# Kernel optimization log

Measured on AMD Instinct MI355X. Metric: run time of the kernel, lower is better.

## Reference

```python
import jax, jax.numpy as jnp
import numpy as np

D, H, DH, DFF, K = 512, 8, 64, 2048, 31
B, T = 8, 1024


def _ln(x, g, b):
    m = x.mean(-1, keepdims=True)
    v = ((x - m) ** 2).mean(-1, keepdims=True)
    return (x - m) / jnp.sqrt(v + 1e-5) * g + b


def _silu(x):
    return x * jax.nn.sigmoid(x)


def _pe(t, d):
    i = jnp.arange(t, dtype=jnp.float32)[:, None]
    j = jnp.arange(0, d, 2, dtype=jnp.float32)
    ang = i * (1.0 / (10000.0 ** (j / d)))
    pe = jnp.zeros((t, d), jnp.float32)
    pe = pe.at[:, 0::2].set(jnp.sin(ang))
    pe = pe.at[:, 1::2].set(jnp.cos(ang))
    return pe


def setup_inputs() -> dict:
    key = jax.random.key(0)
    ks = iter(jax.random.split(key, 40))
    s = 0.02
    d = {
        'x': jax.random.normal(next(ks), (B, T, D), jnp.float32),
        # FF module 1
        'ff1_ln_g': jnp.ones((D,), jnp.float32), 'ff1_ln_b': jnp.zeros((D,), jnp.float32),
        'ff1_w1': jax.random.normal(next(ks), (D, DFF), jnp.float32) * s,
        'ff1_b1': jnp.zeros((DFF,), jnp.float32),
        'ff1_w2': jax.random.normal(next(ks), (DFF, D), jnp.float32) * s,
        'ff1_b2': jnp.zeros((D,), jnp.float32),
        # MHSA
        'mha_ln_g': jnp.ones((D,), jnp.float32), 'mha_ln_b': jnp.zeros((D,), jnp.float32),
        'wq': jax.random.normal(next(ks), (H, D, DH), jnp.float32) * s,
        'bq': jnp.zeros((H, DH), jnp.float32),
        'wk': jax.random.normal(next(ks), (H, D, DH), jnp.float32) * s,
        'bk': jnp.zeros((H, DH), jnp.float32),
        'wv': jax.random.normal(next(ks), (H, D, DH), jnp.float32) * s,
        'bv': jnp.zeros((H, DH), jnp.float32),
        'wo': jax.random.normal(next(ks), (D, D), jnp.float32) * s,
        'bo': jnp.zeros((D,), jnp.float32),
        # Conv module
        'cv_ln_g': jnp.ones((D,), jnp.float32), 'cv_ln_b': jnp.zeros((D,), jnp.float32),
        'cv_w1': jax.random.normal(next(ks), (2 * D, D), jnp.float32) * s,
        'cv_b1': jnp.zeros((2 * D,), jnp.float32),
        'cv_wd': jax.random.normal(next(ks), (D, D, K), jnp.float32) * s,
        'cv_bn_g': jnp.ones((D,), jnp.float32), 'cv_bn_b': jnp.zeros((D,), jnp.float32),
        'cv_w2': jax.random.normal(next(ks), (D, D), jnp.float32) * s,
        'cv_b2': jnp.zeros((D,), jnp.float32),
        # FF module 2
        'ff2_ln_g': jnp.ones((D,), jnp.float32), 'ff2_ln_b': jnp.zeros((D,), jnp.float32),
        'ff2_w1': jax.random.normal(next(ks), (D, DFF), jnp.float32) * s,
        'ff2_b1': jnp.zeros((DFF,), jnp.float32),
        'ff2_w2': jax.random.normal(next(ks), (DFF, D), jnp.float32) * s,
        'ff2_b2': jnp.zeros((D,), jnp.float32),
        # final layer norm
        'fin_g': jnp.ones((D,), jnp.float32), 'fin_b': jnp.zeros((D,), jnp.float32),
    }
    return d


def _block(x, p):
    def ffn(x, g, b, w1, b1, w2, b2):
        y = _silu(_ln(x, g, b) @ w1 + b1) @ w2 + b2
        return x + y  # FeedForwardModule internal residual

    # x = x + 0.5 * ff_1(x)
    x = x + 0.5 * ffn(x, p['ff1_ln_g'], p['ff1_ln_b'], p['ff1_w1'], p['ff1_b1'], p['ff1_w2'], p['ff1_b2'])

    # MHSA module (with its own internal residual), then block residual
    y = _ln(x, p['mha_ln_g'], p['mha_ln_b']) + _pe(x.shape[1], x.shape[2])
    q = jnp.einsum('btd,hde->bhte', y, p['wq']) + p['bq'][None, :, None, :]
    k = jnp.einsum('btd,hde->bhte', y, p['wk']) + p['bk'][None, :, None, :]
    v = jnp.einsum('btd,hde->bhte', y, p['wv']) + p['bv'][None, :, None, :]
    scores = jnp.einsum('bhtd,bhsd->bhts', q, k) * (1.0 / np.sqrt(DH))
    attn = jax.nn.softmax(scores, axis=-1)
    o = jnp.einsum('bhts,bhsd->bhtd', attn, v)
    # faithful to original: raw view [B,H,T,dh] -> [B,T,H*dh] (no transpose)
    o = o.reshape(x.shape[0], x.shape[1], H * DH)
    o = o @ p['wo'] + p['bo']
    x = x + (x + o)

    # Convolution module (internal residual), then block residual
    y = _ln(x, p['cv_ln_g'], p['cv_ln_b']).swapaxes(1, 2)  # [B,D,T]
    y = jnp.einsum('ed,bdt->bet', p['cv_w1'], y) + p['cv_b1'][None, :, None]
    a, g = jnp.split(y, 2, axis=1)
    y = a * jax.nn.sigmoid(g)  # GLU over channel dim
    y = jax.lax.conv_general_dilated(y, p['cv_wd'], (1,), [(K // 2, K // 2)],
                                     dimension_numbers=('NCH', 'OIH', 'NCH'))
    # BatchNorm1d in training mode: batch stats over (batch, time), biased variance
    m = y.mean((0, 2), keepdims=True)
    var = ((y - m) ** 2).mean((0, 2), keepdims=True)
    y = (y - m) / jnp.sqrt(var + 1e-5) * p['cv_bn_g'][None, :, None] + p['cv_bn_b'][None, :, None]
    y = _silu(y)
    y = jnp.einsum('ed,bdt->bet', p['cv_w2'], y) + p['cv_b2'][None, :, None]
    y = y.swapaxes(1, 2)
    x = x + (x + y)

    # x = x + 0.5 * ff_2(x)
    x = x + 0.5 * ffn(x, p['ff2_ln_g'], p['ff2_ln_b'], p['ff2_w1'], p['ff2_b1'], p['ff2_w2'], p['ff2_b2'])

    return _ln(x, p['fin_g'], p['fin_b'])


def reference(x, ff1_ln_g, ff1_ln_b, ff1_w1, ff1_b1, ff1_w2, ff1_b2,
              mha_ln_g, mha_ln_b, wq, bq, wk, bk, wv, bv, wo, bo,
              cv_ln_g, cv_ln_b, cv_w1, cv_b1, cv_wd, cv_bn_g, cv_bn_b, cv_w2, cv_b2,
              ff2_ln_g, ff2_ln_b, ff2_w1, ff2_b1, ff2_w2, ff2_b2,
              fin_g, fin_b):
    p = dict(ff1_ln_g=ff1_ln_g, ff1_ln_b=ff1_ln_b, ff1_w1=ff1_w1, ff1_b1=ff1_b1,
             ff1_w2=ff1_w2, ff1_b2=ff1_b2, mha_ln_g=mha_ln_g, mha_ln_b=mha_ln_b,
             wq=wq, bq=bq, wk=wk, bk=bk, wv=wv, bv=bv, wo=wo, bo=bo,
             cv_ln_g=cv_ln_g, cv_ln_b=cv_ln_b, cv_w1=cv_w1, cv_b1=cv_b1, cv_wd=cv_wd,
             cv_bn_g=cv_bn_g, cv_bn_b=cv_bn_b, cv_w2=cv_w2, cv_b2=cv_b2,
             ff2_ln_g=ff2_ln_g, ff2_ln_b=ff2_ln_b, ff2_w1=ff2_w1, ff2_b1=ff2_b1,
             ff2_w2=ff2_w2, ff2_b2=ff2_b2, fin_g=fin_g, fin_b=fin_b)
    return _block(x, p)
```

## Files before the change

kernel.cpp:

```cpp
#include <hip/hip_runtime.h>


typedef __attribute__((ext_vector_type(4))) float f32x4;
typedef __attribute__((ext_vector_type(8))) short short8;
typedef __attribute__((ext_vector_type(4))) short s16x4;

__device__ __forceinline__ float bfs2f(short s) {
  unsigned u = ((unsigned)(unsigned short)s) << 16;
  float f; __builtin_memcpy(&f, &u, 4); return f;
}
__device__ __forceinline__ short f2bfs(float f) {
  unsigned u; __builtin_memcpy(&u, &f, 4);
  u = (u + 0x7FFFu + ((u >> 16) & 1u)) >> 16;
  return (short)u;
}
__device__ __forceinline__ float sigmoidf_(float x) { return 1.f / (1.f + __expf(-x)); }

#define GLOADLDS(gsrc, ldst) \
  __builtin_amdgcn_global_load_lds((__attribute__((address_space(1))) void*)(gsrc), \
                                   (__attribute__((address_space(3))) void*)(ldst), 16, 0, 0)

#define VMCNT_ASM(n) asm volatile("s_waitcnt vmcnt(" #n ")" ::: "memory")
template<int N> __device__ __forceinline__ void vmcnt_wait() {
  if      constexpr (N == 0)  VMCNT_ASM(0);
  else if constexpr (N == 2)  VMCNT_ASM(2);
  else if constexpr (N == 3)  VMCNT_ASM(3);
  else if constexpr (N == 4)  VMCNT_ASM(4);
  else if constexpr (N == 6)  VMCNT_ASM(6);
  else if constexpr (N == 8)  VMCNT_ASM(8);
  else                        VMCNT_ASM(0);
}
#define MEMFENCE asm volatile("" ::: "memory")

enum { EPI_SILU = 0, EPI_F32BIAS = 1, EPI_RES = 2, EPI_QKV = 3, EPI_F32 = 6 };

template<int BM, int BN, int WM, int WN, int EPI>
__global__ __launch_bounds__(256) void gemm_bt(
    const short* __restrict__ A, int lda, long zAh, long zAl,
    const short* __restrict__ BT, int ldbt, long zBh, long zBl,
    int K, int Kdec,
    void* C, int ldc, long zCh, long zCl, int zdiv,
    const float* bias, const float* bias2, const float* bias3,
    const float* resid, float alpha, float beta)
{
  constexpr int FM = BM / (WM * 16), FN = BN / (WN * 16);
  constexpr int AIT = (BM * 4) / 256, BIT = (BN * 4) / 256;
  constexpr int L = AIT + BIT;
  __shared__ short sA[3][BM * 32];
  __shared__ short sB[3][BN * 32];
  const int tid = threadIdx.x;
  const int zmask = (1 << zdiv) - 1;
  const int zhi = (int)(blockIdx.z >> zdiv);
  const int zlo = (int)(blockIdx.z & zmask);
  A  += (long)zhi * zAh + (long)zlo * zAl;
  BT += (long)zhi * zBh + (long)zlo * zBl;
  char* cbase = (char*)C + (long)zhi * zCh + (long)zlo * zCl;
  const int m0 = blockIdx.x * BM, n0 = blockIdx.y * BN;
  const int Keff = K - (zlo == zmask ? Kdec : 0);

  auto stage = [&](int buf, int k0) {
#pragma unroll
    for (int it = 0; it < AIT; ++it) {
      int idx = it * 256 + tid;
      GLOADLDS(A + (long)(m0 + (idx >> 2)) * lda + k0 + (idx & 3) * 8, &sA[buf][idx * 8]);
    }
#pragma unroll
    for (int it = 0; it < BIT; ++it) {
      int idx = it * 256 + tid;
      GLOADLDS(BT + (long)(n0 + (idx >> 2)) * ldbt + k0 + (idx & 3) * 8, &sB[buf][idx * 8]);
    }
  };

  f32x4 acc[FM][FN];
#pragma unroll
  for (int i = 0; i < FM; ++i) {
#pragma unroll
    for (int j = 0; j < FN; ++j) acc[i][j] = (f32x4){0.f, 0.f, 0.f, 0.f};
  }
  const int lane = tid & 63, wid = tid >> 6;
  const int wm = wid / WN, wn = wid % WN;
  const int lr = lane & 15, kg = lane >> 4;
  const int aRow = wm * (BM / WM), bRow = wn * (BN / WN);

  const int nt = Keff >> 5;
  stage(0, 0);
  stage(1, 32);
  vmcnt_wait<L>();
  __builtin_amdgcn_s_barrier();

  int cur = 0, sbuf = 2;
  for (int t = 0; t < nt; ++t) {
    const bool st = (t + 2 < nt);
    if (st) stage(sbuf, (t + 2) * 32);
    short8 af[FM], bfr[FN];
#pragma unroll
    for (int mi = 0; mi < FM; ++mi)
      af[mi] = *(const short8*)&sA[cur][(aRow + mi * 16 + lr) * 32 + kg * 8];
#pragma unroll
    for (int ni = 0; ni < FN; ++ni)
      bfr[ni] = *(const short8*)&sB[cur][(bRow + ni * 16 + lr) * 32 + kg * 8];
#pragma unroll
    for (int mi = 0; mi < FM; ++mi) {
#pragma unroll
      for (int ni = 0; ni < FN; ++ni)
        acc[mi][ni] = __builtin_amdgcn_mfma_f32_16x16x32_bf16(af[mi], bfr[ni], acc[mi][ni], 0, 0, 0);
    }
    if (st) vmcnt_wait<L>(); else vmcnt_wait<0>();
    __builtin_amdgcn_s_barrier();
    cur = (cur == 2) ? 0 : cur + 1;
    sbuf = (sbuf == 2) ? 0 : sbuf + 1;
  }

  const int baseRow = m0 + aRow, baseCol = n0 + bRow;
#pragma unroll
  for (int mi = 0; mi < FM; ++mi) {
#pragma unroll
    for (int ni = 0; ni < FN; ++ni) {
      const int col = baseCol + ni * 16 + lr;
#pragma unroll
      for (int r = 0; r < 4; ++r) {
        const int row = baseRow + mi * 16 + kg * 4 + r;
        float v = acc[mi][ni][r];
        if (EPI == EPI_SILU) {
          v += bias[col];
          v = v * sigmoidf_(v);
          ((short*)cbase)[(long)row * ldc + col] = f2bfs(v);
        } else if (EPI == EPI_F32BIAS) {
          v += bias[col];
          ((float*)cbase)[(long)row * ldc + col] = v;
        } else if (EPI == EPI_RES) {
          v += bias[col];
          float rv = resid[(long)row * ldc + col];
          ((float*)cbase)[(long)row * ldc + col] = alpha * rv + beta * v;
        } else if (EPI == EPI_QKV) {
          if (col < 512)       v = (v + bias[col]) * 0.125f;
          else if (col < 1024) v += bias2[col - 512];
          else                 v += bias3[col - 1024];
          ((short*)cbase)[(long)row * ldc + col] = f2bfs(v);
        } else if (EPI == EPI_F32) {
          ((float*)cbase)[(long)row * ldc + col] = v;
        }
      }
    }
  }
}

__global__ __launch_bounds__(256) void conv_tap(
    const short* __restrict__ glu,
    const short* __restrict__ wdP,
    float* __restrict__ parts)
{
  __shared__ short sA[2][144 * 32];
  const int tid = threadIdx.x;
  const int bid = blockIdx.x;
  const int cc = bid & 7, j = bid >> 3;
  const int y = cc >> 1, kg = cc & 1;
  const int x = j & 7, b = j >> 3;
  const int m0 = x * 128, n0 = y * 128;
  const short* Arow0 = glu + ((long)b * 1056 + m0 + 1 + kg * 16) * 512;
  float* cbase = parts + (long)kg * (8192L * 512) + (long)b * (1024L * 512);

  const int lane = tid & 63, wid = tid >> 6;
  const int wm = wid >> 1, wn = wid & 1;
  const int lr = lane & 15, kgr = lane >> 4;
  const int aRow = wm * 64, bRow = wn * 64;

  const short* Bp = wdP + (long)((n0 + bRow) >> 4) * (512L * 512)
                  + (long)(kg * 256) * 512 + lane * 8;
  const long NSTR = 512L * 512;

  auto stageA = [&](int buf, int ib) {
#pragma unroll
    for (int it = 0; it < 3; ++it) {
      int idx = it * 256 + tid;
      if (idx < 576) {
        GLOADLDS(Arow0 + (long)(idx >> 2) * 512 + ib * 32 + (idx & 3) * 8,
                 &sA[buf][idx * 8]);
      }
    }
  };

  f32x4 acc[4][4];
#pragma unroll
  for (int i = 0; i < 4; ++i) {
#pragma unroll
    for (int jj = 0; jj < 4; ++jj) acc[i][jj] = (f32x4){0.f, 0.f, 0.f, 0.f};
  }
  short8 b0[4], b1[4];

  stageA(0, 0);
  MEMFENCE;
#pragma unroll
  for (int ni = 0; ni < 4; ++ni)
    b0[ni] = *(const short8*)(Bp + ni * NSTR);
  MEMFENCE;
  vmcnt_wait<4>();
  __builtin_amdgcn_s_barrier();

  int cur = 0;
  for (int ib = 0; ib < 16; ++ib) {
    if (ib + 1 < 16) stageA(cur ^ 1, ib + 1);
    MEMFENCE;
#pragma unroll
    for (int kk = 0; kk < 16; ++kk) {
      const long noff = (kk + 1 < 16) ? (long)((kk + 1) * 16 + ib) * 512
                                      : (long)(ib + 1) * 512;
      if ((kk & 1) == 0) {
#pragma unroll
        for (int ni = 0; ni < 4; ++ni)
          b1[ni] = *(const short8*)(Bp + noff + ni * NSTR);
      } else {
#pragma unroll
        for (int ni = 0; ni < 4; ++ni)
          b0[ni] = *(const short8*)(Bp + noff + ni * NSTR);
      }
      short8 af[4];
#pragma unroll
      for (int mi = 0; mi < 4; ++mi)
        af[mi] = *(const short8*)&sA[cur][(kk + aRow + mi * 16 + lr) * 32 + kgr * 8];
      if ((kk & 1) == 0) {
#pragma unroll
        for (int mi = 0; mi < 4; ++mi) {
#pragma unroll
          for (int ni = 0; ni < 4; ++ni)
            acc[mi][ni] = __builtin_amdgcn_mfma_f32_16x16x32_bf16(af[mi], b0[ni], acc[mi][ni], 0, 0, 0);
        }
      } else {
#pragma unroll
        for (int mi = 0; mi < 4; ++mi) {
#pragma unroll
          for (int ni = 0; ni < 4; ++ni)
            acc[mi][ni] = __builtin_amdgcn_mfma_f32_16x16x32_bf16(af[mi], b1[ni], acc[mi][ni], 0, 0, 0);
        }
      }
    }
    vmcnt_wait<4>();
    __builtin_amdgcn_s_barrier();
    cur ^= 1;
  }
  vmcnt_wait<0>();

  const int baseRow = m0 + aRow, baseCol = n0 + bRow;
#pragma unroll
  for (int mi = 0; mi < 4; ++mi) {
#pragma unroll
    for (int ni = 0; ni < 4; ++ni) {
      const int col = baseCol + ni * 16 + lr;
#pragma unroll
      for (int r = 0; r < 4; ++r) {
        const int row = baseRow + mi * 16 + kgr * 4 + r;
        cbase[(long)row * 512 + col] = acc[mi][ni][r];
      }
    }
  }
}

__global__ __launch_bounds__(256) void flash_attn(
    const short* __restrict__ qkv,
    const short* __restrict__ vt,
    short* __restrict__ out)
{
  __shared__ short sQ[64 * 64];
  __shared__ short sK[64 * 64];
  __shared__ short sV[64 * 64];
  __shared__ short sP[4][16 * 64];
  const int tid = threadIdx.x;
  const int lane = tid & 63, w = tid >> 6;
  const int lr = lane & 15, kg = lane >> 4;
  const int bh = (int)blockIdx.z;
  const int b = bh >> 3, h = bh & 7;
  const int q0 = blockIdx.x * 64;
  const short* qbase = qkv + (long)b * 1024 * 1536 + h * 64;
  const short* kbase = qbase + 512;
  const short* vtb = vt + (long)bh * 65536;

#pragma unroll
  for (int it = 0; it < 2; ++it) {
    int idx = it * 256 + tid;
    int row = idx >> 3, c = (idx & 7) ^ (row & 7);
    GLOADLDS(qbase + (long)(q0 + row) * 1536 + c * 8, &sQ[idx * 8]);
  }
  __syncthreads();
  short8 bq[2];
#pragma unroll
  for (int ks = 0; ks < 2; ++ks)
    bq[ks] = *(const short8*)&sQ[(w * 16 + lr) * 64 + ((ks * 4 + kg) ^ (lr & 7)) * 8];

  f32x4 po[4];
#pragma unroll
  for (int mi = 0; mi < 4; ++mi) po[mi] = (f32x4){0.f, 0.f, 0.f, 0.f};
  float m = -3.0e38f, l = 0.f;

  for (int s0 = 0; s0 < 1024; s0 += 64) {
#pragma unroll
    for (int it = 0; it < 2; ++it) {
      int idx = it * 256 + tid;
      int row = idx >> 3, c = (idx & 7) ^ (row & 7);
      GLOADLDS(kbase + (long)(s0 + row) * 1536 + c * 8, &sK[idx * 8]);
    }
#pragma unroll
    for (int it = 0; it < 2; ++it) {
      int idx = it * 256 + tid;
      int row = idx >> 3, c = (idx & 7) ^ (row & 7);
      GLOADLDS(vtb + (long)row * 1024 + s0 + c * 8, &sV[idx * 8]);
    }
    __syncthreads();

    f32x4 as[4];
#pragma unroll
    for (int mi = 0; mi < 4; ++mi) as[mi] = (f32x4){0.f, 0.f, 0.f, 0.f};
#pragma unroll
    for (int ks = 0; ks < 2; ++ks) {
#pragma unroll
      for (int mi = 0; mi < 4; ++mi) {
        short8 ak = *(const short8*)&sK[(mi * 16 + lr) * 64 + ((ks * 4 + kg) ^ (lr & 7)) * 8];
        as[mi] = __builtin_amdgcn_mfma_f32_16x16x32_bf16(ak, bq[ks], as[mi], 0, 0, 0);
      }
    }

    float rmax = as[0][0];
#pragma unroll
    for (int mi = 0; mi < 4; ++mi) {
#pragma unroll
      for (int r = 0; r < 4; ++r) rmax = fmaxf(rmax, as[mi][r]);
    }
    rmax = fmaxf(rmax, __shfl_xor(rmax, 16));
    rmax = fmaxf(rmax, __shfl_xor(rmax, 32));
    const float mn = fmaxf(m, rmax);
    const float sc = __expf(m - mn);
    float p[4][4];
    float rsum = 0.f;
#pragma unroll
    for (int mi = 0; mi < 4; ++mi) {
#pragma unroll
      for (int r = 0; r < 4; ++r) { p[mi][r] = __expf(as[mi][r] - mn); rsum += p[mi][r]; }
    }
    rsum += __shfl_xor(rsum, 16);
    rsum += __shfl_xor(rsum, 32);
    l = l * sc + rsum;
    m = mn;
#pragma unroll
    for (int mi = 0; mi < 4; ++mi) {
#pragma unroll
      for (int r = 0; r < 4; ++r) po[mi][r] *= sc;
    }
#pragma unroll
    for (int mi = 0; mi < 4; ++mi) {
      s16x4 pk;
#pragma unroll
      for (int r = 0; r < 4; ++r) pk[r] = f2bfs(p[mi][r]);
      *(s16x4*)&sP[w][lr * 64 + ((mi ^ (lr & 3)) * 16 + kg * 4)] = pk;
    }
#pragma unroll
    for (int ks = 0; ks < 2; ++ks) {
      short8 bp = *(const short8*)&sP[w][lr * 64 + (((ks * 2 + (kg >> 1)) ^ (lr & 3)) * 16 + (kg & 1) * 8)];
#pragma unroll
      for (int mi = 0; mi < 4; ++mi) {
        short8 av = *(const short8*)&sV[(mi * 16 + lr) * 64 + ((ks * 4 + kg) ^ (lr & 7)) * 8];
        po[mi] = __builtin_amdgcn_mfma_f32_16x16x32_bf16(av, bp, po[mi], 0, 0, 0);
      }
    }
    __syncthreads();
  }

  const float inv = 1.f / l;
  const int t2 = q0 + w * 16 + lr;
  const int n = h * 1024 + t2;
  short* ob = out + ((long)b * 1024 + (n >> 3)) * 512 + (n & 7) * 64;
#pragma unroll
  for (int mi = 0; mi < 4; ++mi) {
    s16x4 o;
#pragma unroll
    for (int r = 0; r < 4; ++r) o[r] = f2bfs(po[mi][r] * inv);
    *(s16x4*)&ob[mi * 16 + kg * 4] = o;
  }
}

__global__ __launch_bounds__(256) void reduce_bn(
    const float* __restrict__ parts, long pstride,
    short* __restrict__ z, float* stats)
{
  const int r0 = blockIdx.x * 16;
  const int c = threadIdx.x * 2;
  float s0 = 0.f, s1 = 0.f, q0 = 0.f, q1 = 0.f;
#pragma unroll 4
  for (int r = 0; r < 16; ++r) {
    const long idx = (long)(r0 + r) * 512 + c;
    float a0 = parts[idx] + parts[idx + pstride];
    float a1 = parts[idx + 1] + parts[idx + 1 + pstride];
    z[idx] = f2bfs(a0); z[idx + 1] = f2bfs(a1);
    s0 += a0; s1 += a1; q0 += a0 * a0; q1 += a1 * a1;
  }
  atomicAdd(&stats[c], s0);
  atomicAdd(&stats[c + 1], s1);
  atomicAdd(&stats[512 + c], q0);
  atomicAdd(&stats[512 + c + 1], q1);
}

template<int ADDPE, int OUTF32>
__global__ __launch_bounds__(256) void ln_rows(
    const float* __restrict__ X, const float* __restrict__ g, const float* __restrict__ b,
    const float* __restrict__ pe, void* __restrict__ Y)
{
  const int row = blockIdx.x * 4 + (threadIdx.x >> 6);
  const int lane = threadIdx.x & 63;
  const int c0 = lane * 8;
  const float* src = X + (long)row * 512 + c0;
  f32x4 a = *(const f32x4*)src, c = *(const f32x4*)(src + 4);
  float x[8] = {a[0], a[1], a[2], a[3], c[0], c[1], c[2], c[3]};
  float s = 0.f, q = 0.f;
#pragma unroll
  for (int j = 0; j < 8; ++j) { s += x[j]; q += x[j] * x[j]; }
#pragma unroll
  for (int off = 32; off > 0; off >>= 1) { s += __shfl_xor(s, off); q += __shfl_xor(q, off); }
  const float mean = s * (1.f / 512.f);
  const float var = q * (1.f / 512.f) - mean * mean;
  const float rstd = rsqrtf(var + 1e-5f);
  f32x4 g0 = *(const f32x4*)(g + c0), g1 = *(const f32x4*)(g + c0 + 4);
  f32x4 b0 = *(const f32x4*)(b + c0), b1 = *(const f32x4*)(b + c0 + 4);
  float gg[8] = {g0[0], g0[1], g0[2], g0[3], g1[0], g1[1], g1[2], g1[3]};
  float bb[8] = {b0[0], b0[1], b0[2], b0[3], b1[0], b1[1], b1[2], b1[3]};
  float y[8];
#pragma unroll
  for (int j = 0; j < 8; ++j) {
    y[j] = (x[j] - mean) * rstd * gg[j] + bb[j];
    if (ADDPE) y[j] += pe[(long)(row & 1023) * 512 + c0 + j];
  }
  if (OUTF32) {
    float* dst = (float*)Y + (long)row * 512 + c0;
    *(f32x4*)dst = (f32x4){y[0], y[1], y[2], y[3]};
    *(f32x4*)(dst + 4) = (f32x4){y[4], y[5], y[6], y[7]};
  } else {
    short8 o;
#pragma unroll
    for (int j = 0; j < 8; ++j) o[j] = f2bfs(y[j]);
    *(short8*)((short*)Y + (long)row * 512 + c0) = o;
  }
}

template<int INF32>
__global__ __launch_bounds__(256) void transpose64(
    const void* __restrict__ in_, int ldin, short* __restrict__ out, int ldout,
    int ctiles, int zshift, long zh_in, long zl_in, long z_out)
{
  __shared__ short t[64][72];
  const int z = blockIdx.z;
  const long inoff = (long)(z >> zshift) * zh_in + (long)(z & ((1 << zshift) - 1)) * zl_in;
  const int tr = blockIdx.x / ctiles, tc = blockIdx.x % ctiles;
  short* dst = out + (long)z * z_out + (long)(tc * 64) * ldout + tr * 64;
  const int tid = threadIdx.x;
#pragma unroll
  for (int p = 0; p < 2; ++p) {
    int idx = p * 256 + tid;
    int r = idx >> 3, c8 = (idx & 7) * 8;
    if (INF32) {
      const float* src = (const float*)in_ + inoff + (long)(tr * 64 + r) * ldin + tc * 64 + c8;
      f32x4 v0 = *(const f32x4*)src, v1 = *(const f32x4*)(src + 4);
#pragma unroll
      for (int j = 0; j < 4; ++j) { t[r][c8 + j] = f2bfs(v0[j]); t[r][c8 + 4 + j] = f2bfs(v1[j]); }
    } else {
      const short* src = (const short*)in_ + inoff + (long)(tr * 64 + r) * ldin + tc * 64 + c8;
      short8 v = *(const short8*)src;
#pragma unroll
      for (int j = 0; j < 8; ++j) t[r][c8 + j] = v[j];
    }
  }
  __syncthreads();
#pragma unroll
  for (int p = 0; p < 2; ++p) {
    int idx = p * 256 + tid;
    int c = idx >> 3, r8 = (idx & 7) * 8;
    short8 v;
#pragma unroll
    for (int j = 0; j < 8; ++j) v[j] = t[r8 + j][c];
    *(short8*)(dst + (long)c * ldout + r8) = v;
  }
}

__global__ __launch_bounds__(256) void wd_pack(const float* __restrict__ wd, short* __restrict__ wdP)
{
  const int gid = blockIdx.x * 256 + threadIdx.x;
  const int e = gid >> 9, i = gid & 511;
  const float* src = wd + ((long)e * 512 + i) * 31;
  const long rowtile = (long)(e >> 4) * (512L * 512);
  const int inner = ((i >> 3) & 3) * 128 + (e & 15) * 8 + (i & 7);
#pragma unroll
  for (int KK = 0; KK < 31; ++KK)
    wdP[rowtile + (long)(KK * 16 + (i >> 5)) * 512 + inner] = f2bfs(src[KK]);
}

__global__ __launch_bounds__(256) void pe_init(float* __restrict__ pe)
{
  const int gid = blockIdx.x * 256 + threadIdx.x;
  const int t = gid >> 8, p = gid & 255;
  const float freq = __expf(-(float)p * (9.210340371976184f / 256.f));
  const float ang = (float)t * freq;
  pe[(long)t * 512 + 2 * p]     = sinf(ang);
  pe[(long)t * 512 + 2 * p + 1] = cosf(ang);
}

__global__ __launch_bounds__(256) void glu_kernel(const float* __restrict__ y1, short* __restrict__ gp)
{
  const int gid = blockIdx.x * 256 + threadIdx.x;
  const int row = gid >> 7;
  const int ci = (gid & 127) * 4;
  const float* base = y1 + (long)row * 1024;
  f32x4 a = *(const f32x4*)(base + ci);
  f32x4 g = *(const f32x4*)(base + 512 + ci);
  const int b = row >> 10, t = row & 1023;
  s16x4 o;
#pragma unroll
  for (int j = 0; j < 4; ++j) o[j] = f2bfs(a[j] * sigmoidf_(g[j]));
  *(s16x4*)(gp + ((long)b * 1056 + 16 + t) * 512 + ci) = o;
}

__global__ void bn_stats(float* stats, const float* __restrict__ bn_g, const float* __restrict__ bn_b)
{
  const int c = blockIdx.x * 256 + threadIdx.x;
  if (c < 512) {
    float mean = stats[c] * (1.f / 8192.f);
    float var = stats[512 + c] * (1.f / 8192.f) - mean * mean;
    float sc = bn_g[c] * rsqrtf(var + 1e-5f);
    stats[1024 + c] = sc;
    stats[1536 + c] = bn_b[c] - mean * sc;
  }
}

__global__ __launch_bounds__(256) void bn_silu(const short* __restrict__ z, const float* __restrict__ stats,
                                               short* __restrict__ out)
{
  const long base = ((long)blockIdx.x * 256 + threadIdx.x) * 8;
  const int c0 = (int)(base & 511);
  short8 v = *(const short8*)(z + base);
  short8 o;
#pragma unroll
  for (int j = 0; j < 8; ++j) {
    const int c = c0 + j;
    float y = bfs2f(v[j]) * stats[1024 + c] + stats[1536 + c];
    o[j] = f2bfs(y * sigmoidf_(y));
  }
  *(short8*)(out + base) = o;
}

__global__ __launch_bounds__(256) void cast_bf16(const float* __restrict__ in, short* __restrict__ out, long n)
{
  for (long i = (long)blockIdx.x * 256 + threadIdx.x; i < n; i += (long)gridDim.x * 256)
    out[i] = f2bfs(in[i]);
}

extern "C" void kernel_launch(void* const* d_in, const int* in_sizes, int n_in,
                              void* d_out, int out_size, void* d_ws, size_t ws_size,
                              hipStream_t stream)
{
  (void)in_sizes; (void)n_in; (void)out_size; (void)ws_size;
  const float* x_in   = (const float*)d_in[0];
  const float* ff1_g  = (const float*)d_in[1];
  const float* ff1_bb = (const float*)d_in[2];
  const float* ff1_w1 = (const float*)d_in[3];
  const float* ff1_b1 = (const float*)d_in[4];
  const float* ff1_w2 = (const float*)d_in[5];
  const float* ff1_b2 = (const float*)d_in[6];
  const float* mha_g  = (const float*)d_in[7];
  const float* mha_b  = (const float*)d_in[8];
  const float* wq     = (const float*)d_in[9];
  const float* bq     = (const float*)d_in[10];
  const float* wk     = (const float*)d_in[11];
  const float* bk     = (const float*)d_in[12];
  const float* wv     = (const float*)d_in[13];
  const float* bv     = (const float*)d_in[14];
  const float* wo     = (const float*)d_in[15];
  const float* bo     = (const float*)d_in[16];
  const float* cv_g   = (const float*)d_in[17];
  const float* cv_b   = (const float*)d_in[18];
  const float* cv_w1  = (const float*)d_in[19];
  const float* cv_b1  = (const float*)d_in[20];
  const float* cv_wd  = (const float*)d_in[21];
  const float* bn_g   = (const float*)d_in[22];
  const float* bn_b   = (const float*)d_in[23];
  const float* cv_w2  = (const float*)d_in[24];
  const float* cv_b2  = (const float*)d_in[25];
  const float* ff2_g  = (const float*)d_in[26];
  const float* ff2_b  = (const float*)d_in[27];
  const float* ff2_w1 = (const float*)d_in[28];
  const float* ff2_b1 = (const float*)d_in[29];
  const float* ff2_w2 = (const float*)d_in[30];
  const float* ff2_b2 = (const float*)d_in[31];
  const float* fin_g  = (const float*)d_in[32];
  const float* fin_b  = (const float*)d_in[33];

  size_t off = 0;
  char* wsb = (char*)d_ws;
  auto take = [&](size_t n) { char* p = wsb + off; off += (n + 255) & ~(size_t)255; return p; };
  short* ff1w1T = (short*)take(2048L * 512 * 2);
  short* ff1w2T = (short*)take(512L * 2048 * 2);
  short* qkvT   = (short*)take(1536L * 512 * 2);
  short* woT    = (short*)take(512L * 512 * 2);
  short* cw1b   = (short*)take(1024L * 512 * 2);
  short* cw2b   = (short*)take(512L * 512 * 2);
  short* wdP    = (short*)take(32L * 512 * 512 * 2);
  short* ff2w1T = (short*)take(2048L * 512 * 2);
  short* ff2w2T = (short*)take(512L * 2048 * 2);
  float* xcur   = (float*)take(8192L * 512 * 4);
  char*  Ra     = take(8192L * 2048 * 2);
  short* Rb     = (short*)take(8192L * 512 * 2);
  short* Rg     = (short*)take((8L * 1056 + 2) * 512 * 2);
  char*  Rshare = take(2L * 8192 * 512 * 4);
  short* vt     = (short*)take(64L * 64 * 1024 * 2);
  float* pe     = (float*)take(1024L * 512 * 4);
  float* stats  = (float*)take(2048L * 4);

  short* hid = (short*)Ra;
  short* qkv = (short*)Ra;
  float* y1  = (float*)Ra;
  float* part0 = (float*)Rshare;

  transpose64<1><<<dim3(256, 1, 1), 256, 0, stream>>>(ff1_w1, 2048, ff1w1T, 512, 32, 0, 0, 0, 0);
  transpose64<1><<<dim3(256, 1, 1), 256, 0, stream>>>(ff1_w2, 512, ff1w2T, 2048, 8, 0, 0, 0, 0);
  transpose64<1><<<dim3(8, 1, 8), 256, 0, stream>>>(wq, 64, qkvT, 512, 1, 0, 32768, 0, 32768);
  transpose64<1><<<dim3(8, 1, 8), 256, 0, stream>>>(wk, 64, qkvT + 512 * 512, 512, 1, 0, 32768, 0, 32768);
  transpose64<1><<<dim3(8, 1, 8), 256, 0, stream>>>(wv, 64, qkvT + 1024 * 512, 512, 1, 0, 32768, 0, 32768);
  transpose64<1><<<dim3(64, 1, 1), 256, 0, stream>>>(wo, 512, woT, 512, 8, 0, 0, 0, 0);
  transpose64<1><<<dim3(256, 1, 1), 256, 0, stream>>>(ff2_w1, 2048, ff2w1T, 512, 32, 0, 0, 0, 0);
  transpose64<1><<<dim3(256, 1, 1), 256, 0, stream>>>(ff2_w2, 512, ff2w2T, 2048, 8, 0, 0, 0, 0);
  (void)hipMemsetAsync(wdP, 0, 32L * 512 * 512 * 2, stream);
  wd_pack<<<1024, 256, 0, stream>>>(cv_wd, wdP);
  pe_init<<<1024, 256, 0, stream>>>(pe);
  cast_bf16<<<2048, 256, 0, stream>>>(cv_w1, cw1b, 524288L);
  cast_bf16<<<1024, 256, 0, stream>>>(cv_w2, cw2b, 262144L);

  ln_rows<0, 0><<<2048, 256, 0, stream>>>(x_in, ff1_g, ff1_bb, nullptr, Rb);
  gemm_bt<128, 128, 2, 2, EPI_SILU><<<dim3(64, 16, 1), 256, 0, stream>>>(
      Rb, 512, 0, 0, ff1w1T, 512, 0, 0, 512, 0,
      hid, 2048, 0, 0, 0, ff1_b1, nullptr, nullptr, nullptr, 0.f, 0.f);
  gemm_bt<64, 64, 2, 2, EPI_RES><<<dim3(128, 8, 1), 256, 0, stream>>>(
      hid, 2048, 0, 0, ff1w2T, 2048, 0, 0, 2048, 0,
      xcur, 512, 0, 0, 0, ff1_b2, nullptr, nullptr, x_in, 1.5f, 0.5f);

  ln_rows<1, 0><<<2048, 256, 0, stream>>>(xcur, mha_g, mha_b, pe, Rb);
  gemm_bt<128, 128, 2, 2, EPI_QKV><<<dim3(64, 12, 1), 256, 0, stream>>>(
      Rb, 512, 0, 0, qkvT, 512, 0, 0, 512, 0,
      qkv, 1536, 0, 0, 0, bq, bk, bv, nullptr, 0.f, 0.f);
  transpose64<0><<<dim3(16, 1, 64), 256, 0, stream>>>(qkv + 1024, 1536, vt, 1024, 1, 3,
                                                      1024L * 1536, 64, 65536);
  flash_attn<<<dim3(16, 1, 64), 256, 0, stream>>>(qkv, vt, Rb);
  gemm_bt<64, 64, 2, 2, EPI_RES><<<dim3(128, 8, 1), 256, 0, stream>>>(
      Rb, 512, 0, 0, woT, 512, 0, 0, 512, 0,
      xcur, 512, 0, 0, 0, bo, nullptr, nullptr, xcur, 2.f, 1.f);

  ln_rows<0, 0><<<2048, 256, 0, stream>>>(xcur, cv_g, cv_b, nullptr, Rb);
  gemm_bt<128, 128, 2, 2, EPI_F32BIAS><<<dim3(64, 8, 1), 256, 0, stream>>>(
      Rb, 512, 0, 0, cw1b, 512, 0, 0, 512, 0,
      y1, 1024, 0, 0, 0, cv_b1, nullptr, nullptr, nullptr, 0.f, 0.f);
  (void)hipMemsetAsync(Rg, 0, (8L * 1056 + 2) * 512 * 2, stream);
  glu_kernel<<<4096, 256, 0, stream>>>(y1, Rg);
  (void)hipMemsetAsync(stats, 0, 1024 * sizeof(float), stream);
  conv_tap<<<512, 256, 0, stream>>>(Rg, wdP, part0);
  reduce_bn<<<512, 256, 0, stream>>>(part0, 8192L * 512, Rb, stats);
  bn_stats<<<2, 256, 0, stream>>>(stats, bn_g, bn_b);
  bn_silu<<<2048, 256, 0, stream>>>(Rb, stats, (short*)Rg);
  gemm_bt<64, 64, 2, 2, EPI_RES><<<dim3(128, 8, 1), 256, 0, stream>>>(
      (short*)Rg, 512, 0, 0, cw2b, 512, 0, 0, 512, 0,
      xcur, 512, 0, 0, 0, cv_b2, nullptr, nullptr, xcur, 2.f, 1.f);

  ln_rows<0, 0><<<2048, 256, 0, stream>>>(xcur, ff2_g, ff2_b, nullptr, Rb);
  gemm_bt<128, 128, 2, 2, EPI_SILU><<<dim3(64, 16, 1), 256, 0, stream>>>(
      Rb, 512, 0, 0, ff2w1T, 512, 0, 0, 512, 0,
      hid, 2048, 0, 0, 0, ff2_b1, nullptr, nullptr, nullptr, 0.f, 0.f);
  gemm_bt<64, 64, 2, 2, EPI_RES><<<dim3(128, 8, 1), 256, 0, stream>>>(
      hid, 2048, 0, 0, ff2w2T, 2048, 0, 0, 2048, 0,
      xcur, 512, 0, 0, 0, ff2_b2, nullptr, nullptr, xcur, 1.5f, 0.5f);

  ln_rows<0, 1><<<2048, 256, 0, stream>>>(xcur, fin_g, fin_b, nullptr, (float*)d_out);
}
```

Baseline: 547.9 us.

## Store conv partials in bf16, add MFMA priority hints, drop weight-pack memset

The depthwise-as-GEMM conv kernel now writes its two K-split partial sums as bf16 instead of fp32, and the reduction kernel reads and writes packed bf16 pairs. This halves the traffic of the partial buffer. s_setprio raises wave priority around the MFMA blocks in conv_tap and flash_attn. The full memset of the packed conv weights is replaced by writing only the zero padding tap inside wd_pack. Rounding the partials to bf16 before summing adds some precision loss.

```diff
diff --git a/kernel.cpp b/kernel.cpp
--- a/kernel.cpp
+++ b/kernel.cpp
@@ -148,7 +148,7 @@
 __global__ __launch_bounds__(256) void conv_tap(
     const short* __restrict__ glu,
     const short* __restrict__ wdP,
-    float* __restrict__ parts)
+    short* __restrict__ parts)
 {
   __shared__ short sA[2][144 * 32];
   const int tid = threadIdx.x;
@@ -158,7 +158,7 @@
   const int x = j & 7, b = j >> 3;
   const int m0 = x * 128, n0 = y * 128;
   const short* Arow0 = glu + ((long)b * 1056 + m0 + 1 + kg * 16) * 512;
-  float* cbase = parts + (long)kg * (8192L * 512) + (long)b * (1024L * 512);
+  short* cbase = parts + (long)kg * (8192L * 512) + (long)b * (1024L * 512);
 
   const int lane = tid & 63, wid = tid >> 6;
   const int wm = wid >> 1, wn = wid & 1;
@@ -218,6 +218,7 @@
 #pragma unroll
       for (int mi = 0; mi < 4; ++mi)
         af[mi] = *(const short8*)&sA[cur][(kk + aRow + mi * 16 + lr) * 32 + kgr * 8];
+      __builtin_amdgcn_s_setprio(1);
       if ((kk & 1) == 0) {
 #pragma unroll
         for (int mi = 0; mi < 4; ++mi) {
@@ -233,6 +234,7 @@
             acc[mi][ni] = __builtin_amdgcn_mfma_f32_16x16x32_bf16(af[mi], b1[ni], acc[mi][ni], 0, 0, 0);
         }
       }
+      __builtin_amdgcn_s_setprio(0);
     }
     vmcnt_wait<4>();
     __builtin_amdgcn_s_barrier();
@@ -249,7 +251,7 @@
 #pragma unroll
       for (int r = 0; r < 4; ++r) {
         const int row = baseRow + mi * 16 + kgr * 4 + r;
-        cbase[(long)row * 512 + col] = acc[mi][ni][r];
+        cbase[(long)row * 512 + col] = f2bfs(acc[mi][ni][r]);
       }
     }
   }
@@ -309,6 +311,7 @@
     f32x4 as[4];
 #pragma unroll
     for (int mi = 0; mi < 4; ++mi) as[mi] = (f32x4){0.f, 0.f, 0.f, 0.f};
+    __builtin_amdgcn_s_setprio(1);
 #pragma unroll
     for (int ks = 0; ks < 2; ++ks) {
 #pragma unroll
@@ -317,6 +320,7 @@
         as[mi] = __builtin_amdgcn_mfma_f32_16x16x32_bf16(ak, bq[ks], as[mi], 0, 0, 0);
       }
     }
+    __builtin_amdgcn_s_setprio(0);
 
     float rmax = as[0][0];
 #pragma unroll
@@ -351,6 +355,7 @@
       for (int r = 0; r < 4; ++r) pk[r] = f2bfs(p[mi][r]);
       *(s16x4*)&sP[w][lr * 64 + ((mi ^ (lr & 3)) * 16 + kg * 4)] = pk;
     }
+    __builtin_amdgcn_s_setprio(1);
 #pragma unroll
     for (int ks = 0; ks < 2; ++ks) {
       short8 bp = *(const short8*)&sP[w][lr * 64 + (((ks * 2 + (kg >> 1)) ^ (lr & 3)) * 16 + (kg & 1) * 8)];
@@ -360,6 +365,7 @@
         po[mi] = __builtin_amdgcn_mfma_f32_16x16x32_bf16(av, bp, po[mi], 0, 0, 0);
       }
     }
+    __builtin_amdgcn_s_setprio(0);
     __syncthreads();
   }
 
@@ -377,7 +383,7 @@
 }
 
 __global__ __launch_bounds__(256) void reduce_bn(
-    const float* __restrict__ parts, long pstride,
+    const short* __restrict__ parts, long pstride,
     short* __restrict__ z, float* stats)
 {
   const int r0 = blockIdx.x * 16;
@@ -386,9 +392,12 @@
 #pragma unroll 4
   for (int r = 0; r < 16; ++r) {
     const long idx = (long)(r0 + r) * 512 + c;
-    float a0 = parts[idx] + parts[idx + pstride];
-    float a1 = parts[idx + 1] + parts[idx + 1 + pstride];
-    z[idx] = f2bfs(a0); z[idx + 1] = f2bfs(a1);
+    int p0 = *(const int*)&parts[idx];
+    int p1 = *(const int*)&parts[idx + pstride];
+    float a0 = bfs2f((short)(p0 & 0xffff)) + bfs2f((short)(p1 & 0xffff));
+    float a1 = bfs2f((short)(p0 >> 16)) + bfs2f((short)(p1 >> 16));
+    int zo = ((int)(unsigned short)f2bfs(a0)) | (((int)(unsigned short)f2bfs(a1)) << 16);
+    *(int*)&z[idx] = zo;
     s0 += a0; s1 += a1; q0 += a0 * a0; q1 += a1 * a1;
   }
   atomicAdd(&stats[c], s0);
@@ -487,6 +496,7 @@
 #pragma unroll
   for (int KK = 0; KK < 31; ++KK)
     wdP[rowtile + (long)(KK * 16 + (i >> 5)) * 512 + inner] = f2bfs(src[KK]);
+  wdP[rowtile + (long)(31 * 16 + (i >> 5)) * 512 + inner] = 0;
 }
 
 __global__ __launch_bounds__(256) void pe_init(float* __restrict__ pe)
@@ -604,7 +614,7 @@
   char*  Ra     = take(8192L * 2048 * 2);
   short* Rb     = (short*)take(8192L * 512 * 2);
   short* Rg     = (short*)take((8L * 1056 + 2) * 512 * 2);
-  char*  Rshare = take(2L * 8192 * 512 * 4);
+  short* parts  = (short*)take(2L * 8192 * 512 * 2);
   short* vt     = (short*)take(64L * 64 * 1024 * 2);
   float* pe     = (float*)take(1024L * 512 * 4);
   float* stats  = (float*)take(2048L * 4);
@@ -612,7 +622,6 @@
   short* hid = (short*)Ra;
   short* qkv = (short*)Ra;
   float* y1  = (float*)Ra;
-  float* part0 = (float*)Rshare;
 
   transpose64<1><<<dim3(256, 1, 1), 256, 0, stream>>>(ff1_w1, 2048, ff1w1T, 512, 32, 0, 0, 0, 0);
   transpose64<1><<<dim3(256, 1, 1), 256, 0, stream>>>(ff1_w2, 512, ff1w2T, 2048, 8, 0, 0, 0, 0);
@@ -622,7 +631,6 @@
   transpose64<1><<<dim3(64, 1, 1), 256, 0, stream>>>(wo, 512, woT, 512, 8, 0, 0, 0, 0);
   transpose64<1><<<dim3(256, 1, 1), 256, 0, stream>>>(ff2_w1, 2048, ff2w1T, 512, 32, 0, 0, 0, 0);
   transpose64<1><<<dim3(256, 1, 1), 256, 0, stream>>>(ff2_w2, 512, ff2w2T, 2048, 8, 0, 0, 0, 0);
-  (void)hipMemsetAsync(wdP, 0, 32L * 512 * 512 * 2, stream);
   wd_pack<<<1024, 256, 0, stream>>>(cv_wd, wdP);
   pe_init<<<1024, 256, 0, stream>>>(pe);
   cast_bf16<<<2048, 256, 0, stream>>>(cv_w1, cw1b, 524288L);
@@ -654,8 +662,8 @@
   (void)hipMemsetAsync(Rg, 0, (8L * 1056 + 2) * 512 * 2, stream);
   glu_kernel<<<4096, 256, 0, stream>>>(y1, Rg);
   (void)hipMemsetAsync(stats, 0, 1024 * sizeof(float), stream);
-  conv_tap<<<512, 256, 0, stream>>>(Rg, wdP, part0);
-  reduce_bn<<<512, 256, 0, stream>>>(part0, 8192L * 512, Rb, stats);
+  conv_tap<<<512, 256, 0, stream>>>(Rg, wdP, parts);
+  reduce_bn<<<512, 256, 0, stream>>>(parts, 8192L * 512, Rb, stats);
   bn_stats<<<2, 256, 0, stream>>>(stats, bn_g, bn_b);
   bn_silu<<<2048, 256, 0, stream>>>(Rb, stats, (short*)Rg);
   gemm_bt<64, 64, 2, 2, EPI_RES><<<dim3(128, 8, 1), 256, 0, stream>>>(
```

Result: faster. 508.0 us (-7.3%).
